# Performance work log

Measured on AMD Instinct MI355X. Metric: run time of the kernel, lower is better.

## Reference

```python
import jax, jax.numpy as jnp
import numpy as np

# hardcoded constants from the source module
C = 768      # n_embd
H = 8        # n_head
HS = C // H  # head_size = 96
E = 8        # n_experts
K = 2        # top_k
L = 12       # n_layer
V = 95       # vocab_size = len(chars)
BS = 64      # block_size
B, T = 16, 64


def setup_inputs() -> dict:
    key = jax.random.key(0)
    ks = iter(jax.random.split(key, 32))
    nrm = lambda shape: jax.random.normal(next(ks), shape, dtype=jnp.float32) * 0.02
    d = {
        'idx': jax.random.randint(next(ks), (B, T), 0, V),
        'tok_emb': nrm((V, C)),
        'pos_emb': nrm((BS, C)),
        # attention (per-layer stacked); per-head q/k/v linears concatenated into [C, C]
        'Wq': nrm((L, C, C)), 'Wk': nrm((L, C, C)), 'Wv': nrm((L, C, C)),
        'Wo': nrm((L, C, C)), 'bo': jnp.zeros((L, C), jnp.float32),
        # MoE
        'gate_W': nrm((L, C, E)), 'gate_b': jnp.zeros((L, E), jnp.float32),
        'W1': nrm((L, E, C, 4 * C)), 'b1': jnp.zeros((L, E, 4 * C), jnp.float32),
        'W2': nrm((L, E, 4 * C, C)), 'b2': jnp.zeros((L, E, C), jnp.float32),
        # layernorms
        'ln1_g': jnp.ones((L, C), jnp.float32), 'ln1_b': jnp.zeros((L, C), jnp.float32),
        'ln2_g': jnp.ones((L, C), jnp.float32), 'ln2_b': jnp.zeros((L, C), jnp.float32),
        'lnf_g': jnp.ones((C,), jnp.float32), 'lnf_b': jnp.zeros((C,), jnp.float32),
        # lm head
        'head_W': nrm((C, V)), 'head_b': jnp.zeros((V,), jnp.float32),
    }
    return d


def _layernorm(x, g, b, eps=1e-5):
    mu = x.mean(-1, keepdims=True)
    var = ((x - mu) ** 2).mean(-1, keepdims=True)
    return (x - mu) * jax.lax.rsqrt(var + eps) * g + b


def _moe(x, gw, gb, w1, b1, w2, b2):
    # x: [B,T,C]; compute all experts densely then combine top-k (faithful to source)
    xf = x.reshape(-1, C)                                  # [N,C]
    probs = jax.nn.softmax(xf @ gw + gb, axis=-1)          # [N,E]
    tp, ti = jax.lax.top_k(probs, K)                       # [N,K]
    tp = tp / tp.sum(-1, keepdims=True)
    h = jax.nn.gelu(jnp.einsum('nc,ech->neh', xf, w1) + b1, approximate=False)
    eo = jnp.einsum('neh,ehc->nec', h, w2) + b2            # [N,E,C]
    sel = jnp.take_along_axis(eo, ti[:, :, None], axis=1)  # [N,K,C]
    return (tp[:, :, None] * sel).sum(1).reshape(x.shape)


def _forward(idx, tok_emb, pos_emb, Wq, Wk, Wv, Wo, bo, gate_W, gate_b, W1, b1,
             W2, b2, ln1_g, ln1_b, ln2_g, ln2_b, lnf_g, lnf_b, head_W, head_b):
    Bc, Tc = idx.shape
    x = tok_emb[idx] + pos_emb[jnp.arange(Tc) % BS]        # [B,T,C]
    mask = jnp.tril(jnp.ones((Tc, Tc), bool))

    def block(x, p):
        q = (x @ p['Wq']).reshape(Bc, Tc, H, HS)
        k = (x @ p['Wk']).reshape(Bc, Tc, H, HS)
        v = (x @ p['Wv']).reshape(Bc, Tc, H, HS)
        att = jnp.einsum('bqhd,bkhd->bhqk', q, k) * (HS ** -0.5)
        att = jnp.where(mask, att, -jnp.inf)
        w = jax.nn.softmax(att, axis=-1)
        o = jnp.einsum('bhqk,bkhd->bqhd', w, v).reshape(Bc, Tc, C)
        y = o @ p['Wo'] + p['bo']
        x = _layernorm(x + y, p['g1'], p['b1n'])
        y = _moe(x, p['gw'], p['gb'], p['w1'], p['bb1'], p['w2'], p['bb2'])
        x = _layernorm(x + y, p['g2'], p['b2n'])
        return x, None

    params = {'Wq': Wq, 'Wk': Wk, 'Wv': Wv, 'Wo': Wo, 'bo': bo,
              'gw': gate_W, 'gb': gate_b, 'w1': W1, 'bb1': b1, 'w2': W2, 'bb2': b2,
              'g1': ln1_g, 'b1n': ln1_b, 'g2': ln2_g, 'b2n': ln2_b}
    x, _ = jax.lax.scan(block, x, params)
    x = _layernorm(x, lnf_g, lnf_b)
    return x @ head_W + head_b                              # [B,T,V]


def reference(idx, tok_emb, pos_emb, Wq, Wk, Wv, Wo, bo, gate_W, gate_b, W1, b1,
              W2, b2, ln1_g, ln1_b, ln2_g, ln2_b, lnf_g, lnf_b, head_W, head_b):
    return _forward(idx, tok_emb, pos_emb, Wq, Wk, Wv, Wo, bo, gate_W, gate_b,
                    W1, b1, W2, b2, ln1_g, ln1_b, ln2_g, ln2_b, lnf_g, lnf_b,
                    head_W, head_b)
```

## Files before the change

### kernel.cpp

```cpp
#include <hip/hip_runtime.h>
#include <math.h>

#define C    768
#define HN   8
#define HS   96
#define NE   8
#define NL   12
#define NV   95
#define TT   64
#define NB   16
#define NTOK 1024
#define H4   3072
#define NKR  2048
#define NKRP 2176
#define MC   (NTOK * C)

typedef __attribute__((ext_vector_type(8))) short short8;
typedef __attribute__((ext_vector_type(4))) float floatx4;

union U16x8 { uint4 u; short8 s; };
static __device__ __forceinline__ short8 as_s8(uint4 u) { U16x8 x; x.u = u; return x.s; }
static __device__ __forceinline__ uint4 ror16x4(uint4 q) {
  uint4 r;
  r.x = (q.x >> 16) | (q.x << 16);
  r.y = (q.y >> 16) | (q.y << 16);
  r.z = (q.z >> 16) | (q.z << 16);
  r.w = (q.w >> 16) | (q.w << 16);
  return r;
}

static __device__ __forceinline__ unsigned pack_split(float f) {
  unsigned u = __float_as_uint(f);
  unsigned h = (u + 0x7fffu + ((u >> 16) & 1u)) >> 16;
  float d = f - __uint_as_float(h << 16);
  unsigned v = __float_as_uint(d);
  unsigned l = (v + 0x7fffu + ((v >> 16) & 1u)) >> 16;
  return h | (l << 16);
}
static __device__ __forceinline__ float unpack_split(unsigned w) {
  return __uint_as_float(w << 16) + __uint_as_float(w & 0xffff0000u);
}

static __device__ __forceinline__ void gload_lds16(const unsigned* g, unsigned* l) {
  __builtin_amdgcn_global_load_lds(
      (const __attribute__((address_space(1))) unsigned*)g,
      (__attribute__((address_space(3))) unsigned*)l, 16, 0, 0);
}

__global__ void __launch_bounds__(256) k_prep(const float* __restrict__ src,
    unsigned* __restrict__ dst, int K, int N, long matStride, long dstMatStride) {
  int nt = blockIdx.x, kt = blockIdx.y, mz = blockIdx.z;
  const float* W = src + (size_t)mz * matStride;
  unsigned* out = dst + (size_t)mz * dstMatStride
                + ((size_t)nt * (K >> 5) + kt) * 4096;
  __shared__ float ls[32 * 130];
  int tid = threadIdx.x;
  int n0 = nt * 128, k0 = kt * 32;
  #pragma unroll
  for (int p = 0; p < 16; ++p) {
    int idx = p * 256 + tid;
    int k = idx >> 7, c = idx & 127;
    int n = n0 + c;
    ls[k * 130 + c] = (n < N) ? W[(size_t)(k0 + k) * N + n] : 0.f;
  }
  __syncthreads();
  #pragma unroll
  for (int p = 0; p < 16; ++p) {
    int idx = p * 256 + tid;
    int col = idx >> 5, ks = idx & 31;
    int k = ks ^ ((col & 7) << 2);
    out[idx] = pack_split(ls[k * 130 + col]);
  }
}

template<int OUTMODE>
static __device__ __forceinline__ void gemm_body(
    const unsigned* __restrict__ Ap, const int* __restrict__ perm,
    const unsigned* __restrict__ Wt, const float* __restrict__ bias,
    float* __restrict__ outF, unsigned* __restrict__ outP,
    int row0, int Mend, int col0, int N, int K, int kbeg, int kend)
{
  __shared__ __align__(16) unsigned Bt[2][64 * 32];
  const int tid  = threadIdx.x;
  const int lane = tid & 63, wv = tid >> 6;
  const int l16  = lane & 15, lq = lane >> 4;
  const int sw   = (l16 & 7) << 2;

  int ra0 = row0 + wv * 32 + l16;
  int ra1 = ra0 + 16;
  if (ra0 > Mend - 1) ra0 = Mend - 1;
  if (ra1 > Mend - 1) ra1 = Mend - 1;
  if (perm) { ra0 = perm[ra0]; ra1 = perm[ra1]; }
  const unsigned* A0 = Ap + (size_t)ra0 * K;
  const unsigned* A1 = Ap + (size_t)ra1 * K;

  const unsigned* tsrc = Wt + ((size_t)(col0 >> 7) * (K >> 5) + (kbeg >> 5)) * 4096
                       + ((size_t)((col0 >> 6) & 1)) * 2048;
  auto stageB = [&](int buf, int kt) {
    const unsigned* s = tsrc + (size_t)kt * 4096 + wv * 512 + lane * 4;
    unsigned* d = &Bt[buf][wv * 512 + lane * 4];
    gload_lds16(s, d);
    gload_lds16(s + 256, d + 256);
  };

  uint4 ac0[2], ac1[2];
  auto loadA = [&](int kpos, uint4* d0, uint4* d1) {
    const unsigned* p = A0 + kpos;
    d0[0] = *(const uint4*)(p + lq * 4);
    d0[1] = *(const uint4*)(p + 16 + lq * 4);
    p = A1 + kpos;
    d1[0] = *(const uint4*)(p + lq * 4);
    d1[1] = *(const uint4*)(p + 16 + lq * 4);
  };

  floatx4 acc[2][4];
  #pragma unroll
  for (int h = 0; h < 2; ++h)
    #pragma unroll
    for (int f = 0; f < 4; ++f) acc[h][f] = (floatx4){0, 0, 0, 0};

  const int ns = (kend - kbeg) >> 5;
  stageB(0, 0);
  loadA(kbeg, ac0, ac1);

  for (int s = 0; s < ns; ++s) {
    const int b = s & 1;
    __syncthreads();
    if (s + 1 < ns) stageB(b ^ 1, s + 1);
    const int kn = kbeg + ((s + 1 < ns) ? (s + 1) * 32 : s * 32);
    uint4 na0[2], na1[2];
    loadA(kn, na0, na1);
    const unsigned* bp = Bt[b];
    #pragma unroll
    for (int f = 0; f < 4; ++f) {
      const unsigned* base = bp + (f * 16 + l16) * 32;
      uint4 q0 = *(const uint4*)(base + ((4 * lq) ^ sw));
      uint4 q1 = *(const uint4*)(base + ((16 + 4 * lq) ^ sw));
      short8 b0 = as_s8(q0), b0r = as_s8(ror16x4(q0));
      short8 b1 = as_s8(q1), b1r = as_s8(ror16x4(q1));
      short8 a00 = as_s8(ac0[0]), a01 = as_s8(ac0[1]);
      short8 a10 = as_s8(ac1[0]), a11 = as_s8(ac1[1]);
      acc[0][f] = __builtin_amdgcn_mfma_f32_16x16x32_bf16(a00, b0,  acc[0][f], 0, 0, 0);
      acc[1][f] = __builtin_amdgcn_mfma_f32_16x16x32_bf16(a10, b0,  acc[1][f], 0, 0, 0);
      acc[0][f] = __builtin_amdgcn_mfma_f32_16x16x32_bf16(a00, b0r, acc[0][f], 0, 0, 0);
      acc[1][f] = __builtin_amdgcn_mfma_f32_16x16x32_bf16(a10, b0r, acc[1][f], 0, 0, 0);
      acc[0][f] = __builtin_amdgcn_mfma_f32_16x16x32_bf16(a01, b1,  acc[0][f], 0, 0, 0);
      acc[1][f] = __builtin_amdgcn_mfma_f32_16x16x32_bf16(a11, b1,  acc[1][f], 0, 0, 0);
      acc[0][f] = __builtin_amdgcn_mfma_f32_16x16x32_bf16(a01, b1r, acc[0][f], 0, 0, 0);
      acc[1][f] = __builtin_amdgcn_mfma_f32_16x16x32_bf16(a11, b1r, acc[1][f], 0, 0, 0);
    }
    ac0[0] = na0[0]; ac0[1] = na0[1]; ac1[0] = na1[0]; ac1[1] = na1[1];
  }

  const int rb = row0 + wv * 32 + lq * 4;
  #pragma unroll
  for (int h = 0; h < 2; ++h) {
    #pragma unroll
    for (int f = 0; f < 4; ++f) {
      int cc = col0 + f * 16 + l16;
      if (cc < N) {
        float bb = (OUTMODE == 1) ? bias[cc] : 0.f;
        #pragma unroll
        for (int r = 0; r < 4; ++r) {
          int rr = rb + h * 16 + r;
          if (rr < Mend) {
            float v = acc[h][f][r] + bb;
            if (OUTMODE == 1) {
              v = 0.5f * v * (1.f + erff(v * 0.70710678118654752f));
              outP[(size_t)rr * N + cc] = pack_split(v);
            } else {
              outF[(size_t)rr * N + cc] = v;
            }
          }
        }
      }
    }
  }
}

static __device__ __forceinline__ void expert_range(const int* counts, int e,
                                                    int& off, int& cnt) {
  off = 0; cnt = 0;
  #pragma unroll
  for (int i = 0; i < NE; ++i) {
    int c = counts[i];
    if (i < e) off += c;
    if (i == e) cnt = c;
  }
}

__global__ void __launch_bounds__(256, 2) k_qkv(const unsigned* xp, const unsigned* Wq,
    const unsigned* Wk, const unsigned* Wv, float* qkvp) {
  int z = blockIdx.z, mat = z >> 1, ch = z & 1;
  const unsigned* W = mat == 0 ? Wq : (mat == 1 ? Wk : Wv);
  gemm_body<2>(xp, nullptr, W, nullptr, qkvp + (size_t)z * MC, nullptr,
               blockIdx.y * 128, NTOK, blockIdx.x * 64, C, C, ch * 384, (ch + 1) * 384);
}

__global__ void __launch_bounds__(256, 2) k_wo(const unsigned* op, const unsigned* W,
    float* wop) {
  int ch = blockIdx.z;
  gemm_body<2>(op, nullptr, W, nullptr, wop + (size_t)ch * MC, nullptr,
               blockIdx.y * 128, NTOK, blockIdx.x * 64, C, C, ch * 128, (ch + 1) * 128);
}

__global__ void __launch_bounds__(256, 2) k_w1(const unsigned* xp, const int* perm,
    const unsigned* W1, const float* b1, unsigned* Hgp, const int* counts) {
  int e = blockIdx.z, off, cnt;
  expert_range(counts, e, off, cnt);
  int r0 = blockIdx.y * 128;
  if (r0 >= cnt) return;
  gemm_body<1>(xp, perm, W1 + (size_t)e * C * H4, b1 + (size_t)e * H4, nullptr, Hgp,
               off + r0, off + cnt, blockIdx.x * 64, H4, C, 0, C);
}

__global__ void __launch_bounds__(256, 2) k_w2(const unsigned* Hgp, const unsigned* W2,
    float* Ypart, const int* counts) {
  int z = blockIdx.z, e = z >> 2, ch = z & 3;
  int off, cnt;
  expert_range(counts, e, off, cnt);
  int r0 = blockIdx.y * 128;
  if (r0 >= cnt) return;
  gemm_body<2>(Hgp, nullptr, W2 + (size_t)e * H4 * C, nullptr,
               Ypart + (size_t)ch * NKRP * C, nullptr,
               off + r0, off + cnt, blockIdx.x * 64, C, H4, ch * 768, (ch + 1) * 768);
}

__global__ void __launch_bounds__(256, 2) k_head(const unsigned* xp, const unsigned* W,
    float* hpart) {
  int ch = blockIdx.z;
  gemm_body<2>(xp, nullptr, W, nullptr, hpart + (size_t)ch * NTOK * NV, nullptr,
               blockIdx.y * 128, NTOK, blockIdx.x * 64, NV, C, ch * 64, (ch + 1) * 64);
}

__global__ void k_headsum(const float* hpart, const float* headb, float* out) {
  int n = blockIdx.x, c = threadIdx.x;
  if (c < NV) {
    size_t i = (size_t)n * NV + c;
    float s = headb[c];
    #pragma unroll
    for (int ch = 0; ch < 12; ++ch) s += hpart[i + (size_t)ch * NTOK * NV];
    out[i] = s;
  }
}

__global__ void k_embed(const int* __restrict__ idx, const float* __restrict__ tok,
                        const float* __restrict__ pos, unsigned* __restrict__ xp) {
  int n = blockIdx.x; int t = n & (TT - 1);
  int token = idx[n];
  for (int j = threadIdx.x; j < C; j += 256)
    xp[(size_t)n * C + j] = pack_split(tok[(size_t)token * C + j] + pos[(size_t)t * C + j]);
}

static __device__ __forceinline__ void ln_finish(int tid, float* v, const float* g,
                                                 const float* bb, unsigned* outrow,
                                                 float* sp) {
  int lane = tid & 63, wid = tid >> 6;
  float s = v[0] + v[1] + v[2];
  for (int o = 32; o; o >>= 1) s += __shfl_down(s, o);
  if (!lane) sp[wid] = s;
  __syncthreads();
  float mean = (sp[0] + sp[1] + sp[2] + sp[3]) * (1.f / C);
  __syncthreads();
  float d0 = v[0] - mean, d1 = v[1] - mean, d2 = v[2] - mean;
  float qq = d0 * d0 + d1 * d1 + d2 * d2;
  for (int o = 32; o; o >>= 1) qq += __shfl_down(qq, o);
  if (!lane) sp[wid] = qq;
  __syncthreads();
  float var = (sp[0] + sp[1] + sp[2] + sp[3]) * (1.f / C);
  float rs = rsqrtf(var + 1e-5f);
  #pragma unroll
  for (int i = 0; i < 3; ++i) {
    int c = tid + i * 256;
    v[i] = (v[i] - mean) * rs * g[c] + bb[c];
    outrow[c] = pack_split(v[i]);
  }
}

__global__ void __launch_bounds__(256) k_ln1g(unsigned* __restrict__ xp,
    const float* __restrict__ wop, const float* __restrict__ bo,
    const float* __restrict__ g, const float* __restrict__ bb,
    const float* __restrict__ gW, const float* __restrict__ gb,
    int* __restrict__ ti, float* __restrict__ tp, int* __restrict__ pos,
    int* __restrict__ counts) {
  int n = blockIdx.x; int tid = threadIdx.x;
  __shared__ float sp[4];
  __shared__ float gs[4][NE];
  float v[3];
  #pragma unroll
  for (int i = 0; i < 3; ++i) {
    int c = tid + i * 256;
    size_t gi = (size_t)n * C + c;
    float acc = unpack_split(xp[gi]) + bo[c];
    #pragma unroll
    for (int ch = 0; ch < 6; ++ch) acc += wop[gi + (size_t)ch * MC];
    v[i] = acc;
  }
  ln_finish(tid, v, g, bb, xp + (size_t)n * C, sp);
  float a[NE];
  #pragma unroll
  for (int e = 0; e < NE; ++e) a[e] = 0.f;
  #pragma unroll
  for (int i = 0; i < 3; ++i) {
    int c = tid + i * 256;
    const float* gr = gW + (size_t)c * NE;
    #pragma unroll
    for (int e = 0; e < NE; ++e) a[e] += v[i] * gr[e];
  }
  int lane = tid & 63, wid = tid >> 6;
  #pragma unroll
  for (int e = 0; e < NE; ++e)
    for (int o = 32; o; o >>= 1) a[e] += __shfl_down(a[e], o);
  if (!lane)
    #pragma unroll
    for (int e = 0; e < NE; ++e) gs[wid][e] = a[e];
  __syncthreads();
  if (tid == 0) {
    float p[NE]; float m = -1e30f;
    #pragma unroll
    for (int e = 0; e < NE; ++e) {
      p[e] = gs[0][e] + gs[1][e] + gs[2][e] + gs[3][e] + gb[e];
      m = fmaxf(m, p[e]);
    }
    float den = 0.f;
    #pragma unroll
    for (int e = 0; e < NE; ++e) { p[e] = expf(p[e] - m); den += p[e]; }
    float inv = 1.f / den;
    #pragma unroll
    for (int e = 0; e < NE; ++e) p[e] *= inv;
    int e0 = 0;
    for (int e = 1; e < NE; ++e) if (p[e] > p[e0]) e0 = e;
    int e1 = -1;
    for (int e = 0; e < NE; ++e) if (e != e0 && (e1 < 0 || p[e] > p[e1])) e1 = e;
    float ss = p[e0] + p[e1];
    int p0 = atomicAdd(&counts[e0], 1), p1 = atomicAdd(&counts[e1], 1);
    ti[n * 2] = e0;  ti[n * 2 + 1] = e1;
    pos[n * 2] = p0; pos[n * 2 + 1] = p1;
    tp[n * 2] = p[e0] / ss; tp[n * 2 + 1] = p[e1] / ss;
  }
}

__global__ void k_perm(const int* __restrict__ ti, const int* __restrict__ pos,
                       const int* __restrict__ counts, int* __restrict__ rowOf,
                       int* __restrict__ perm) {
  int a = blockIdx.x * 256 + threadIdx.x;
  if (a >= NKRP) return;
  if (a >= NKR) { perm[a] = 0; return; }
  int e = ti[a];
  int off = 0;
  #pragma unroll
  for (int i = 0; i < NE; ++i) if (i < e) off += counts[i];
  int row = off + pos[a];
  rowOf[a] = row;
  perm[row] = a >> 1;
}

__global__ void __launch_bounds__(256) k_ln_moe(unsigned* __restrict__ xp,
    const float* __restrict__ Ypart, const int* __restrict__ rowOf,
    const int* __restrict__ ti, const float* __restrict__ tp,
    const float* __restrict__ b2, const float* __restrict__ g,
    const float* __restrict__ bb) {
  int n = blockIdx.x; int tid = threadIdx.x;
  __shared__ float sp[4];
  int r0 = rowOf[n * 2], r1 = rowOf[n * 2 + 1];
  int e0 = ti[n * 2], e1 = ti[n * 2 + 1];
  float w0 = tp[n * 2], w1 = tp[n * 2 + 1];
  const float* bz0 = b2 + (size_t)e0 * C;
  const float* bz1 = b2 + (size_t)e1 * C;
  float v[3];
  #pragma unroll
  for (int i = 0; i < 3; ++i) {
    int c = tid + i * 256;
    float y0 = bz0[c], y1 = bz1[c];
    #pragma unroll
    for (int ch = 0; ch < 4; ++ch) {
      const float* pl = Ypart + (size_t)ch * NKRP * C;
      y0 += pl[(size_t)r0 * C + c];
      y1 += pl[(size_t)r1 * C + c];
    }
    v[i] = unpack_split(xp[(size_t)n * C + c]) + w0 * y0 + w1 * y1;
  }
  ln_finish(tid, v, g, bb, xp + (size_t)n * C, sp);
}

__global__ void __launch_bounds__(256) k_lnf(unsigned* __restrict__ xp,
    const float* __restrict__ g, const float* __restrict__ bb) {
  int n = blockIdx.x; int tid = threadIdx.x;
  __shared__ float sp[4];
  float v[3];
  #pragma unroll
  for (int i = 0; i < 3; ++i) v[i] = unpack_split(xp[(size_t)n * C + tid + i * 256]);
  ln_finish(tid, v, g, bb, xp + (size_t)n * C, sp);
}

__global__ void __launch_bounds__(256) k_attn(const float* __restrict__ qkvp,
    unsigned* __restrict__ op, int* __restrict__ counts) {
  int bh = blockIdx.x; int b = bh >> 3, h = bh & 7;
  int tid = threadIdx.x;
  if (bh == 0 && tid < NE) counts[tid] = 0;
  __shared__ float qs[TT][HS];
  __shared__ float kv[TT][HS];
  const float* q0 = qkvp;                  const float* q1 = qkvp + MC;
  const float* k0 = qkvp + 2 * (size_t)MC; const float* k1 = qkvp + 3 * (size_t)MC;
  const float* v0 = qkvp + 4 * (size_t)MC; const float* v1 = qkvp + 5 * (size_t)MC;
  for (int i = tid; i < TT * HS; i += 256) {
    int t = i / HS, d = i % HS;
    size_t gi = (size_t)(b * TT + t) * C + h * HS + d;
    qs[t][d] = q0[gi] + q1[gi];
    kv[t][d] = k0[gi] + k1[gi];
  }
  __syncthreads();
  int r = tid >> 2, g = tid & 3;
  const float scale = 0.10206207261596575f;
  float sreg[16];
  {
    const floatx4* q4 = (const floatx4*)&qs[r][0];
    #pragma unroll
    for (int j = 0; j < 16; ++j) {
      int kk = g * 16 + j;
      float s = -1e30f;
      if (kk <= r) {
        const floatx4* k4 = (const floatx4*)&kv[kk][0];
        float a2 = 0.f;
        #pragma unroll
        for (int d4 = 0; d4 < HS / 4; ++d4) {
          floatx4 a = q4[d4], bbv = k4[d4];
          a2 += a[0]*bbv[0] + a[1]*bbv[1] + a[2]*bbv[2] + a[3]*bbv[3];
        }
        s = a2 * scale;
      }
      sreg[j] = s;
    }
  }
  float m = sreg[0];
  #pragma unroll
  for (int j = 1; j < 16; ++j) m = fmaxf(m, sreg[j]);
  m = fmaxf(m, __shfl_xor(m, 1));
  m = fmaxf(m, __shfl_xor(m, 2));
  float den = 0.f;
  #pragma unroll
  for (int j = 0; j < 16; ++j) { sreg[j] = expf(sreg[j] - m); den += sreg[j]; }
  den += __shfl_xor(den, 1);
  den += __shfl_xor(den, 2);
  float inv = 1.f / den;
  __syncthreads();
  float (*psc)[TT] = (float(*)[TT])&qs[0][0];
  #pragma unroll
  for (int j = 0; j < 16; ++j) psc[r][g * 16 + j] = sreg[j] * inv;
  for (int i = tid; i < TT * HS; i += 256) {
    int t = i / HS, d = i % HS;
    size_t gi = (size_t)(b * TT + t) * C + h * HS + d;
    kv[t][d] = v0[gi] + v1[gi];
  }
  __syncthreads();
  floatx4 accv[6];
  #pragma unroll
  for (int cc = 0; cc < 6; ++cc) accv[cc] = (floatx4){0, 0, 0, 0};
  for (int kk = 0; kk < TT; ++kk) {
    float wgt = psc[r][kk];
    const floatx4* v4 = (const floatx4*)&kv[kk][0];
    #pragma unroll
    for (int cc = 0; cc < 6; ++cc) accv[cc] += wgt * v4[g * 6 + cc];
  }
  unsigned* orow = op + (size_t)(b * TT + r) * C + h * HS + g * 24;
  #pragma unroll
  for (int cc = 0; cc < 6; ++cc)
    #pragma unroll
    for (int mm = 0; mm < 4; ++mm) orow[cc * 4 + mm] = pack_split(accv[cc][mm]);
}

extern "C" void kernel_launch(void* const* d_in, const int* in_sizes, int n_in,
                              void* d_out, int out_size, void* d_ws, size_t ws_size,
                              hipStream_t stream) {
  const int*   idx   = (const int*)d_in[0];
  const float* tok   = (const float*)d_in[1];
  const float* pose  = (const float*)d_in[2];
  const float* Wq    = (const float*)d_in[3];
  const float* Wk    = (const float*)d_in[4];
  const float* Wv    = (const float*)d_in[5];
  const float* Wo    = (const float*)d_in[6];
  const float* bo    = (const float*)d_in[7];
  const float* gW    = (const float*)d_in[8];
  const float* gb    = (const float*)d_in[9];
  const float* W1    = (const float*)d_in[10];
  const float* b1    = (const float*)d_in[11];
  const float* W2    = (const float*)d_in[12];
  const float* b2    = (const float*)d_in[13];
  const float* ln1g  = (const float*)d_in[14];
  const float* ln1b  = (const float*)d_in[15];
  const float* ln2g  = (const float*)d_in[16];
  const float* ln2b  = (const float*)d_in[17];
  const float* lnfg  = (const float*)d_in[18];
  const float* lnfb  = (const float*)d_in[19];
  const float* headW = (const float*)d_in[20];
  const float* headb = (const float*)d_in[21];
  float* out = (float*)d_out;

  if (ws_size < (size_t)2200 * 1024 * 1024) return;
  char* w = (char*)d_ws;
  auto allocU = [&](size_t n) { unsigned* p = (unsigned*)w; w += n * 4; return p; };
  auto allocF = [&](size_t n) { float* p = (float*)w; w += n * 4; return p; };
  unsigned* Wqp = allocU((size_t)NL * C * C);
  unsigned* Wkp = allocU((size_t)NL * C * C);
  unsigned* Wvp = allocU((size_t)NL * C * C);
  unsigned* Wop = allocU((size_t)NL * C * C);
  unsigned* W1p = allocU((size_t)NL * NE * C * H4);
  unsigned* W2p = allocU((size_t)NL * NE * H4 * C);
  unsigned* Whp = allocU((size_t)24 * 4096);
  unsigned* xp    = allocU((size_t)MC);
  unsigned* op    = allocU((size_t)MC);
  float*    qkvp  = allocF((size_t)6 * MC);
  float*    wop   = allocF((size_t)6 * MC);
  unsigned* Hgp   = allocU((size_t)NKRP * H4);
  float*    Ypart = allocF((size_t)4 * NKRP * C);
  float*    hpart = allocF((size_t)12 * NTOK * NV);
  float*    tp    = allocF(NKR);
  int* ti     = (int*)w; w += NKR * 4;
  int* posA   = (int*)w; w += NKR * 4;
  int* rowOf  = (int*)w; w += NKR * 4;
  int* perm   = (int*)w; w += NKRP * 4;
  int* counts = (int*)w; w += NE * 4;

  k_prep<<<dim3(6, 24, 12), 256, 0, stream>>>(Wq, Wqp, C, C, (long)C * C, (long)C * C);
  k_prep<<<dim3(6, 24, 12), 256, 0, stream>>>(Wk, Wkp, C, C, (long)C * C, (long)C * C);
  k_prep<<<dim3(6, 24, 12), 256, 0, stream>>>(Wv, Wvp, C, C, (long)C * C, (long)C * C);
  k_prep<<<dim3(6, 24, 12), 256, 0, stream>>>(Wo, Wop, C, C, (long)C * C, (long)C * C);
  k_prep<<<dim3(24, 24, 96), 256, 0, stream>>>(W1, W1p, C, H4, (long)C * H4, (long)C * H4);
  k_prep<<<dim3(6, 96, 96), 256, 0, stream>>>(W2, W2p, H4, C, (long)H4 * C, (long)H4 * C);
  k_prep<<<dim3(1, 24, 1), 256, 0, stream>>>(headW, Whp, C, NV, 0, 0);

  k_embed<<<NTOK, 256, 0, stream>>>(idx, tok, pose, xp);

  for (int l = 0; l < NL; ++l) {
    k_qkv<<<dim3(12, 8, 6), 256, 0, stream>>>(
        xp, Wqp + (size_t)l * C * C, Wkp + (size_t)l * C * C, Wvp + (size_t)l * C * C, qkvp);
    k_attn<<<NB * HN, 256, 0, stream>>>(qkvp, op, counts);
    k_wo<<<dim3(12, 8, 6), 256, 0, stream>>>(op, Wop + (size_t)l * C * C, wop);
    k_ln1g<<<NTOK, 256, 0, stream>>>(xp, wop, bo + (size_t)l * C,
        ln1g + (size_t)l * C, ln1b + (size_t)l * C,
        gW + (size_t)l * C * NE, gb + (size_t)l * NE, ti, tp, posA, counts);
    k_perm<<<(NKRP + 255) / 256, 256, 0, stream>>>(ti, posA, counts, rowOf, perm);
    k_w1<<<dim3(48, 8, 8), 256, 0, stream>>>(xp, perm,
        W1p + (size_t)l * NE * C * H4, b1 + (size_t)l * NE * H4, Hgp, counts);
    k_w2<<<dim3(12, 8, 32), 256, 0, stream>>>(Hgp,
        W2p + (size_t)l * NE * H4 * C, Ypart, counts);
    k_ln_moe<<<NTOK, 256, 0, stream>>>(xp, Ypart, rowOf, ti, tp,
        b2 + (size_t)l * NE * C, ln2g + (size_t)l * C, ln2b + (size_t)l * C);
  }

  k_lnf<<<NTOK, 256, 0, stream>>>(xp, lnfg, lnfb);
  k_head<<<dim3(2, 8, 12), 256, 0, stream>>>(xp, Whp, hpart);
  k_headsum<<<NTOK, 128, 0, stream>>>(hpart, headb, out);
}
```

Measured before the change: 4.105 ms.

## Widen GEMM k-step to 128 with fewer barriers, XCD swizzle, resize split-K grids

The shared GEMM body now stages four 32-wide k-slices of B per buffer (128 per step), so it hits a barrier four times less often. A operands are loaded straight from global inside the inner loop instead of being prefetched. A block-index swizzle spreads consecutive blocks across the eight XCDs. Split-K for Wo and the LM head drops to 2 chunks, which shrinks the partial-sum buffers and the reduction loops. The W1/W2 grids double in y to cover more rows per expert. The larger LDS footprint (64KB per block) may cut occupancy, and losing the A prefetch may expose global load latency.

After: 4.355 ms. 6.1% more time.

```diff
diff --git a/kernel.cpp b/kernel.cpp
--- a/kernel.cpp
+++ b/kernel.cpp
@@ -47,6 +47,14 @@
       (__attribute__((address_space(3))) unsigned*)l, 16, 0, 0);
 }
 
+static __device__ __forceinline__ void xcd_swz(int& bx, int& by, int& bz) {
+  int gx = gridDim.x, gy = gridDim.y;
+  int n = gx * gy * (int)gridDim.z;
+  int id = bx + gx * (by + gy * bz);
+  id = (id & 7) * (n >> 3) + (id >> 3);
+  bx = id % gx; int r = id / gx; by = r % gy; bz = r / gy;
+}
+
 __global__ void __launch_bounds__(256) k_prep(const float* __restrict__ src,
     unsigned* __restrict__ dst, int K, int N, long matStride, long dstMatStride) {
   int nt = blockIdx.x, kt = blockIdx.y, mz = blockIdx.z;
@@ -80,7 +88,7 @@
     float* __restrict__ outF, unsigned* __restrict__ outP,
     int row0, int Mend, int col0, int N, int K, int kbeg, int kend)
 {
-  __shared__ __align__(16) unsigned Bt[2][64 * 32];
+  __shared__ __align__(16) unsigned Bt[2][4 * 2048];
   const int tid  = threadIdx.x;
   const int lane = tid & 63, wv = tid >> 6;
   const int l16  = lane & 15, lq = lane >> 4;
@@ -96,60 +104,57 @@
 
   const unsigned* tsrc = Wt + ((size_t)(col0 >> 7) * (K >> 5) + (kbeg >> 5)) * 4096
                        + ((size_t)((col0 >> 6) & 1)) * 2048;
-  auto stageB = [&](int buf, int kt) {
-    const unsigned* s = tsrc + (size_t)kt * 4096 + wv * 512 + lane * 4;
-    unsigned* d = &Bt[buf][wv * 512 + lane * 4];
-    gload_lds16(s, d);
-    gload_lds16(s + 256, d + 256);
+  auto stageB = [&](int buf, int step) {
+    #pragma unroll
+    for (int ss = 0; ss < 4; ++ss) {
+      const unsigned* s = tsrc + (size_t)(step * 4 + ss) * 4096 + wv * 512 + lane * 4;
+      unsigned* d = &Bt[buf][ss * 2048 + wv * 512 + lane * 4];
+      gload_lds16(s, d);
+      gload_lds16(s + 256, d + 256);
+    }
   };
 
-  uint4 ac0[2], ac1[2];
-  auto loadA = [&](int kpos, uint4* d0, uint4* d1) {
-    const unsigned* p = A0 + kpos;
-    d0[0] = *(const uint4*)(p + lq * 4);
-    d0[1] = *(const uint4*)(p + 16 + lq * 4);
-    p = A1 + kpos;
-    d1[0] = *(const uint4*)(p + lq * 4);
-    d1[1] = *(const uint4*)(p + 16 + lq * 4);
-  };
-
   floatx4 acc[2][4];
   #pragma unroll
   for (int h = 0; h < 2; ++h)
     #pragma unroll
     for (int f = 0; f < 4; ++f) acc[h][f] = (floatx4){0, 0, 0, 0};
 
-  const int ns = (kend - kbeg) >> 5;
+  const int ns = (kend - kbeg) >> 7;
   stageB(0, 0);
-  loadA(kbeg, ac0, ac1);
 
   for (int s = 0; s < ns; ++s) {
     const int b = s & 1;
     __syncthreads();
     if (s + 1 < ns) stageB(b ^ 1, s + 1);
-    const int kn = kbeg + ((s + 1 < ns) ? (s + 1) * 32 : s * 32);
-    uint4 na0[2], na1[2];
-    loadA(kn, na0, na1);
     const unsigned* bp = Bt[b];
     #pragma unroll
-    for (int f = 0; f < 4; ++f) {
-      const unsigned* base = bp + (f * 16 + l16) * 32;
-      uint4 q0 = *(const uint4*)(base + ((4 * lq) ^ sw));
-      uint4 q1 = *(const uint4*)(base + ((16 + 4 * lq) ^ sw));
-      short8 b0 = as_s8(q0), b0r = as_s8(ror16x4(q0));
-      short8 b1 = as_s8(q1), b1r = as_s8(ror16x4(q1));
-      short8 a00 = as_s8(ac0[0]), a01 = as_s8(ac0[1]);
-      short8 a10 = as_s8(ac1[0]), a11 = as_s8(ac1[1]);
-      acc[0][f] = __builtin_amdgcn_mfma_f32_16x16x32_bf16(a00, b0,  acc[0][f], 0, 0, 0);
-      acc[1][f] = __builtin_amdgcn_mfma_f32_16x16x32_bf16(a10, b0,  acc[1][f], 0, 0, 0);
-      acc[0][f] = __builtin_amdgcn_mfma_f32_16x16x32_bf16(a00, b0r, acc[0][f], 0, 0, 0);
-      acc[1][f] = __builtin_amdgcn_mfma_f32_16x16x32_bf16(a10, b0r, acc[1][f], 0, 0, 0);
-      acc[0][f] = __builtin_amdgcn_mfma_f32_16x16x32_bf16(a01, b1,  acc[0][f], 0, 0, 0);
-      acc[1][f] = __builtin_amdgcn_mfma_f32_16x16x32_bf16(a11, b1,  acc[1][f], 0, 0, 0);
-      acc[0][f] = __builtin_amdgcn_mfma_f32_16x16x32_bf16(a01, b1r, acc[0][f], 0, 0, 0);
-      acc[1][f] = __builtin_amdgcn_mfma_f32_16x16x32_bf16(a11, b1r, acc[1][f], 0, 0, 0);
+    for (int ss = 0; ss < 4; ++ss) {
+      const int koff = kbeg + s * 128 + ss * 32;
+      uint4 a00 = *(const uint4*)(A0 + koff + lq * 4);
+      uint4 a01 = *(const uint4*)(A0 + koff + 16 + lq * 4);
+      uint4 a10 = *(const uint4*)(A1 + koff + lq * 4);
+      uint4 a11 = *(const uint4*)(A1 + koff + 16 + lq * 4);
+      const unsigned* bsub = bp + ss * 2048;
+      #pragma unroll
+      for (int f = 0; f < 4; ++f) {
+        const unsigned* base = bsub + (f * 16 + l16) * 32;
+        uint4 q0 = *(const uint4*)(base + ((4 * lq) ^ sw));
+        uint4 q1 = *(const uint4*)(base + ((16 + 4 * lq) ^ sw));
+        short8 b0 = as_s8(q0), b0r = as_s8(ror16x4(q0));
+        short8 b1 = as_s8(q1), b1r = as_s8(ror16x4(q1));
+        short8 a00s = as_s8(a00), a01s = as_s8(a01);
+        short8 a10s = as_s8(a10), a11s = as_s8(a11);
+        acc[0][f] = __builtin_amdgcn_mfma_f32_16x16x32_bf16(a00s, b0,  acc[0][f], 0, 0, 0);
+        acc[1][f] = __builtin_amdgcn_mfma_f32_16x16x32_bf16(a10s, b0,  acc[1][f], 0, 0, 0);
+        acc[0][f] = __builtin_amdgcn_mfma_f32_16x16x32_bf16(a00s, b0r, acc[0][f], 0, 0, 0);
+        acc[1][f] = __builtin_amdgcn_mfma_f32_16x16x32_bf16(a10s, b0r, acc[1][f], 0, 0, 0);
+        acc[0][f] = __builtin_amdgcn_mfma_f32_16x16x32_bf16(a01s, b1,  acc[0][f], 0, 0, 0);
+        acc[1][f] = __builtin_amdgcn_mfma_f32_16x16x32_bf16(a11s, b1,  acc[1][f], 0, 0, 0);
+        acc[0][f] = __builtin_amdgcn_mfma_f32_16x16x32_bf16(a01s, b1r, acc[0][f], 0, 0, 0);
+        acc[1][f] = __builtin_amdgcn_mfma_f32_16x16x32_bf16(a11s, b1r, acc[1][f], 0, 0, 0);
+      }
     }
-    ac0[0] = na0[0]; ac0[1] = na0[1]; ac1[0] = na1[0]; ac1[1] = na1[1];
   }
 
   const int rb = row0 + wv * 32 + lq * 4;
@@ -191,46 +196,53 @@
 
 __global__ void __launch_bounds__(256, 2) k_qkv(const unsigned* xp, const unsigned* Wq,
     const unsigned* Wk, const unsigned* Wv, float* qkvp) {
-  int z = blockIdx.z, mat = z >> 1, ch = z & 1;
+  int bx = blockIdx.x, by = blockIdx.y, bz = blockIdx.z;
+  xcd_swz(bx, by, bz);
+  int mat = bz >> 1, ch = bz & 1;
   const unsigned* W = mat == 0 ? Wq : (mat == 1 ? Wk : Wv);
-  gemm_body<2>(xp, nullptr, W, nullptr, qkvp + (size_t)z * MC, nullptr,
-               blockIdx.y * 128, NTOK, blockIdx.x * 64, C, C, ch * 384, (ch + 1) * 384);
+  gemm_body<2>(xp, nullptr, W, nullptr, qkvp + (size_t)bz * MC, nullptr,
+               by * 128, NTOK, bx * 64, C, C, ch * 384, (ch + 1) * 384);
 }
 
 __global__ void __launch_bounds__(256, 2) k_wo(const unsigned* op, const unsigned* W,
     float* wop) {
-  int ch = blockIdx.z;
-  gemm_body<2>(op, nullptr, W, nullptr, wop + (size_t)ch * MC, nullptr,
-               blockIdx.y * 128, NTOK, blockIdx.x * 64, C, C, ch * 128, (ch + 1) * 128);
+  int bx = blockIdx.x, by = blockIdx.y, bz = blockIdx.z;
+  xcd_swz(bx, by, bz);
+  gemm_body<2>(op, nullptr, W, nullptr, wop + (size_t)bz * MC, nullptr,
+               by * 128, NTOK, bx * 64, C, C, bz * 384, (bz + 1) * 384);
 }
 
 __global__ void __launch_bounds__(256, 2) k_w1(const unsigned* xp, const int* perm,
     const unsigned* W1, const float* b1, unsigned* Hgp, const int* counts) {
-  int e = blockIdx.z, off, cnt;
+  int bx = blockIdx.x, by = blockIdx.y, bz = blockIdx.z;
+  xcd_swz(bx, by, bz);
+  int e = bz, off, cnt;
   expert_range(counts, e, off, cnt);
-  int r0 = blockIdx.y * 128;
+  int r0 = by * 128;
   if (r0 >= cnt) return;
   gemm_body<1>(xp, perm, W1 + (size_t)e * C * H4, b1 + (size_t)e * H4, nullptr, Hgp,
-               off + r0, off + cnt, blockIdx.x * 64, H4, C, 0, C);
+               off + r0, off + cnt, bx * 64, H4, C, 0, C);
 }
 
 __global__ void __launch_bounds__(256, 2) k_w2(const unsigned* Hgp, const unsigned* W2,
     float* Ypart, const int* counts) {
-  int z = blockIdx.z, e = z >> 2, ch = z & 3;
+  int bx = blockIdx.x, by = blockIdx.y, bz = blockIdx.z;
+  xcd_swz(bx, by, bz);
+  int e = bz >> 2, ch = bz & 3;
   int off, cnt;
   expert_range(counts, e, off, cnt);
-  int r0 = blockIdx.y * 128;
+  int r0 = by * 128;
   if (r0 >= cnt) return;
   gemm_body<2>(Hgp, nullptr, W2 + (size_t)e * H4 * C, nullptr,
                Ypart + (size_t)ch * NKRP * C, nullptr,
-               off + r0, off + cnt, blockIdx.x * 64, C, H4, ch * 768, (ch + 1) * 768);
+               off + r0, off + cnt, bx * 64, C, H4, ch * 768, (ch + 1) * 768);
 }
 
 __global__ void __launch_bounds__(256, 2) k_head(const unsigned* xp, const unsigned* W,
     float* hpart) {
   int ch = blockIdx.z;
   gemm_body<2>(xp, nullptr, W, nullptr, hpart + (size_t)ch * NTOK * NV, nullptr,
-               blockIdx.y * 128, NTOK, blockIdx.x * 64, NV, C, ch * 64, (ch + 1) * 64);
+               blockIdx.y * 128, NTOK, blockIdx.x * 64, NV, C, ch * 384, (ch + 1) * 384);
 }
 
 __global__ void k_headsum(const float* hpart, const float* headb, float* out) {
@@ -239,7 +251,7 @@
     size_t i = (size_t)n * NV + c;
     float s = headb[c];
     #pragma unroll
-    for (int ch = 0; ch < 12; ++ch) s += hpart[i + (size_t)ch * NTOK * NV];
+    for (int ch = 0; ch < 2; ++ch) s += hpart[i + (size_t)ch * NTOK * NV];
     out[i] = s;
   }
 }
@@ -293,7 +305,7 @@
     size_t gi = (size_t)n * C + c;
     float acc = unpack_split(xp[gi]) + bo[c];
     #pragma unroll
-    for (int ch = 0; ch < 6; ++ch) acc += wop[gi + (size_t)ch * MC];
+    for (int ch = 0; ch < 2; ++ch) acc += wop[gi + (size_t)ch * MC];
     v[i] = acc;
   }
   ln_finish(tid, v, g, bb, xp + (size_t)n * C, sp);
@@ -510,10 +522,10 @@
   unsigned* xp    = allocU((size_t)MC);
   unsigned* op    = allocU((size_t)MC);
   float*    qkvp  = allocF((size_t)6 * MC);
-  float*    wop   = allocF((size_t)6 * MC);
+  float*    wop   = allocF((size_t)2 * MC);
   unsigned* Hgp   = allocU((size_t)NKRP * H4);
   float*    Ypart = allocF((size_t)4 * NKRP * C);
-  float*    hpart = allocF((size_t)12 * NTOK * NV);
+  float*    hpart = allocF((size_t)2 * NTOK * NV);
   float*    tp    = allocF(NKR);
   int* ti     = (int*)w; w += NKR * 4;
   int* posA   = (int*)w; w += NKR * 4;
@@ -535,20 +547,20 @@
     k_qkv<<<dim3(12, 8, 6), 256, 0, stream>>>(
         xp, Wqp + (size_t)l * C * C, Wkp + (size_t)l * C * C, Wvp + (size_t)l * C * C, qkvp);
     k_attn<<<NB * HN, 256, 0, stream>>>(qkvp, op, counts);
-    k_wo<<<dim3(12, 8, 6), 256, 0, stream>>>(op, Wop + (size_t)l * C * C, wop);
+    k_wo<<<dim3(12, 8, 2), 256, 0, stream>>>(op, Wop + (size_t)l * C * C, wop);
     k_ln1g<<<NTOK, 256, 0, stream>>>(xp, wop, bo + (size_t)l * C,
         ln1g + (size_t)l * C, ln1b + (size_t)l * C,
         gW + (size_t)l * C * NE, gb + (size_t)l * NE, ti, tp, posA, counts);
     k_perm<<<(NKRP + 255) / 256, 256, 0, stream>>>(ti, posA, counts, rowOf, perm);
-    k_w1<<<dim3(48, 8, 8), 256, 0, stream>>>(xp, perm,
+    k_w1<<<dim3(48, 16, 8), 256, 0, stream>>>(xp, perm,
         W1p + (size_t)l * NE * C * H4, b1 + (size_t)l * NE * H4, Hgp, counts);
-    k_w2<<<dim3(12, 8, 32), 256, 0, stream>>>(Hgp,
+    k_w2<<<dim3(12, 16, 32), 256, 0, stream>>>(Hgp,
         W2p + (size_t)l * NE * H4 * C, Ypart, counts);
     k_ln_moe<<<NTOK, 256, 0, stream>>>(xp, Ypart, rowOf, ti, tp,
         b2 + (size_t)l * NE * C, ln2g + (size_t)l * C, ln2b + (size_t)l * C);
   }
 
   k_lnf<<<NTOK, 256, 0, stream>>>(xp, lnfg, lnfb);
-  k_head<<<dim3(2, 8, 12), 256, 0, stream>>>(xp, Whp, hpart);
+  k_head<<<dim3(2, 8, 2), 256, 0, stream>>>(xp, Whp, hpart);
   k_headsum<<<NTOK, 128, 0, stream>>>(hpart, headb, out);
 }
```
